# Performance work log

Hardware: AMD Instinct MI355X
Metric: run time of the kernel (lower is better)

## Reference

```python
import jax, jax.numpy as jnp
import numpy as np

EPS = 1e-6


def setup_inputs() -> dict:
    key = jax.random.key(0)
    kx, ky = jax.random.split(key)
    B, C, H, W = 8, 128, 48, 64
    x = jax.random.normal(kx, (B, C, H, W), dtype=jnp.float32)
    y = jax.random.normal(ky, (B, C, H, W), dtype=jnp.float32)
    return {"x": x, "y": y}


def reference(x, y):
    # x, y: (b, c, h, w)
    b, c, h, w = x.shape
    # torch: x.transpose(2,3).view(b,c,h*w) -> x flattened w-major,
    #        so output channel k = v*h + u corresponds to x[:, :, u, v].
    # corr5[b, v, u, i, j] = sum_c x[b,c,u,v] * y[b,c,i,j]
    corr = jnp.einsum('bcuv,bcij->bvuij', x, y)
    corr = corr.reshape(b, w * h, h, w)  # channel k = v*h + u
    # normalization: ReLU then L2-normalize over the h*w channel dim
    corr = jax.nn.relu(corr)
    norm = jnp.sqrt(jnp.sum(corr * corr, axis=1, keepdims=True) + EPS)
    return corr / norm
```

## Files before the change

### kernel.cpp

```cpp
#include <hip/hip_runtime.h>
#include <hip/hip_bf16.h>

#define NB 8
#define NC 128
#define NH 48
#define NW 64
#define NS 3072
#define EPSF 1e-6f

#define GLOBAL_AS __attribute__((address_space(1)))
#define LDS_AS __attribute__((address_space(3)))

typedef __bf16 bf16x8 __attribute__((ext_vector_type(8)));
typedef float f32x4 __attribute__((ext_vector_type(4)));

__device__ __forceinline__ unsigned short bf16_rtne(float f) {
  union { float f; unsigned u; } c;
  c.f = f;
  unsigned r = (c.u + 0x7fffu + ((c.u >> 16) & 1u)) >> 16;
  return (unsigned short)r;
}

__global__ __launch_bounds__(256) void transpose_both(
    const float* __restrict__ x, const float* __restrict__ y,
    __hip_bfloat16* __restrict__ AT, __hip_bfloat16* __restrict__ BT) {
  __shared__ float tile[32 * 129];
  const int id = blockIdx.x;
  const int b = id & 7;
  const int which = (id >> 3) & 1;
  const int f0 = (id >> 4) * 32;
  const float* src = which ? y : x;
  __hip_bfloat16* dst = which ? BT : AT;
  const int t = threadIdx.x;

  {
    const int fl = (t & 7) * 4, cg0 = t >> 3;
    const float* sp = src + (size_t)b * NC * NS + f0 + fl;
#pragma unroll
    for (int i = 0; i < 4; ++i) {
      int cg = cg0 + i * 32;
      f32x4 v = *(const f32x4*)(sp + (size_t)cg * NS);
      tile[(fl + 0) * 129 + cg] = v[0];
      tile[(fl + 1) * 129 + cg] = v[1];
      tile[(fl + 2) * 129 + cg] = v[2];
      tile[(fl + 3) * 129 + cg] = v[3];
    }
  }
  __syncthreads();
  {
    const int c4 = (t & 31) * 4, kl0 = t >> 5;
    unsigned short* dp = (unsigned short*)dst;
#pragma unroll
    for (int i = 0; i < 4; ++i) {
      int fl = kl0 + i * 8;
      int f = f0 + fl;
      int k = which ? f : ((f & 63) * NH + (f >> 6));
      f32x4 v = *(const f32x4*)&tile[fl * 129 + c4];
      ushort4 u4;
      u4.x = bf16_rtne(v[0]);
      u4.y = bf16_rtne(v[1]);
      u4.z = bf16_rtne(v[2]);
      u4.w = bf16_rtne(v[3]);
      *(ushort4*)(dp + ((size_t)b * NS + k) * NC + c4) = u4;
    }
  }
}

template <int CPW>
__device__ __forceinline__ void stage_tile(const char* gsrc, char* ldst,
                                           int wid, int lane) {
  const int lr = lane >> 4, lg = lane & 15;
#pragma unroll
  for (int i = 0; i < CPW; ++i) {
    int c = wid * CPW + i;
    int row = c * 4 + lr;
    int g = lg ^ (row & 7);
    __builtin_amdgcn_global_load_lds(
        (const GLOBAL_AS unsigned*)(gsrc + row * 256 + g * 16),
        (LDS_AS unsigned*)(ldst + c * 1024), 16, 0, 0);
  }
}

__global__ __launch_bounds__(256, 2) void corr_part_v2(
    const __hip_bfloat16* __restrict__ AT,
    const __hip_bfloat16* __restrict__ BT, float* __restrict__ part) {
  __shared__ char smem[65536];
  char* As = smem;
  char* Bs = smem + 32768;
  const int id = blockIdx.x;
  const int b = id & 7;
  const int tl = id >> 3;
  const int nt = tl >> 3;
  const int mg = tl & 7;
  const int t = threadIdx.x;
  const int lane = t & 63, wid = t >> 6;
  const int wm = wid >> 1, wn = wid & 1;
  const int l15 = lane & 15, kg = lane >> 4;

  const char* Ab = (const char*)(AT + ((size_t)b * NS + mg * 384) * NC);
  const char* Bg = (const char*)(BT + ((size_t)b * NS + nt * 128) * NC);

  stage_tile<8>(Bg, Bs, wid, lane);

  float cs[4] = {0.f, 0.f, 0.f, 0.f};
  const int rx = l15 & 7;
#pragma unroll 1
  for (int i = 0; i < 3; ++i) {
    stage_tile<8>(Ab + (size_t)i * 32768, As, wid, lane);
    asm volatile("s_waitcnt vmcnt(0)" ::: "memory");
    __builtin_amdgcn_sched_barrier(0);
    __builtin_amdgcn_s_barrier();

    f32x4 acc[4][4] = {};
#pragma unroll
    for (int kk = 0; kk < 4; ++kk) {
      int g = (kk * 4 + kg) ^ rx;
      bf16x8 a[4], bb[4];
#pragma unroll
      for (int mi = 0; mi < 4; ++mi)
        a[mi] = *(const bf16x8*)(As + (wm * 64 + mi * 16 + l15) * 256 + g * 16);
#pragma unroll
      for (int ni = 0; ni < 4; ++ni)
        bb[ni] =
            *(const bf16x8*)(Bs + (wn * 64 + ni * 16 + l15) * 256 + g * 16);
#pragma unroll
      for (int mi = 0; mi < 4; ++mi)
#pragma unroll
        for (int ni = 0; ni < 4; ++ni)
          acc[mi][ni] = __builtin_amdgcn_mfma_f32_16x16x32_bf16(
              a[mi], bb[ni], acc[mi][ni], 0, 0, 0);
    }
#pragma unroll
    for (int ni = 0; ni < 4; ++ni)
#pragma unroll
      for (int mi = 0; mi < 4; ++mi)
#pragma unroll
        for (int r = 0; r < 4; ++r) {
          float v = fmaxf(acc[mi][ni][r], 0.f);
          cs[ni] += v * v;
        }
    __builtin_amdgcn_s_barrier();
  }

#pragma unroll
  for (int ni = 0; ni < 4; ++ni) {
    cs[ni] += __shfl_xor(cs[ni], 16, 64);
    cs[ni] += __shfl_xor(cs[ni], 32, 64);
  }
  float* csum = (float*)smem;
  if (kg == 0) {
#pragma unroll
    for (int ni = 0; ni < 4; ++ni)
      csum[wm * 128 + wn * 64 + ni * 16 + l15] = cs[ni];
  }
  __syncthreads();
  if (t < 128) {
    float s = csum[t] + csum[128 + t];
    part[(size_t)mg * (NB * NS) + (size_t)b * NS + nt * 128 + t] = s;
  }
}

__global__ __launch_bounds__(256, 2) void corr_out(
    const __hip_bfloat16* __restrict__ AT,
    const __hip_bfloat16* __restrict__ BT, const float* __restrict__ part_in,
    float* __restrict__ out) {
  __shared__ char smem[66560];
  float* rnc = (float*)(smem + 65536);
  const int id = blockIdx.x;
  const int b = id & 7;
  const int tl = id >> 3;
  const int mt = tl / 24, nt = tl - mt * 24;
  const int t = threadIdx.x;
  const int lane = t & 63, wid = t >> 6;
  const int wm = wid >> 1, wn = wid & 1;
  const int l15 = lane & 15, kg = lane >> 4;

  const char* Ag = (const char*)(AT + ((size_t)b * NS + mt * 128) * NC);
  const char* Bg = (const char*)(BT + ((size_t)b * NS + nt * 128) * NC);
  stage_tile<8>(Ag, smem, wid, lane);
  stage_tile<8>(Bg, smem + 32768, wid, lane);
  if (t < 128) {
    float s = 0.f;
#pragma unroll
    for (int q = 0; q < 8; ++q)
      s += part_in[(size_t)q * (NB * NS) + (size_t)b * NS + nt * 128 + t];
    rnc[t] = rsqrtf(s + EPSF);
  }
  __syncthreads();

  f32x4 acc[4][4] = {};
  const int rx = l15 & 7;
#pragma unroll
  for (int kk = 0; kk < 4; ++kk) {
    int g = (kk * 4 + kg) ^ rx;
    bf16x8 a[4], bb[4];
#pragma unroll
    for (int mi = 0; mi < 4; ++mi)
      a[mi] = *(const bf16x8*)(smem + (wm * 64 + mi * 16 + l15) * 256 + g * 16);
#pragma unroll
    for (int ni = 0; ni < 4; ++ni)
      bb[ni] = *(const bf16x8*)(smem + 32768 +
                                (wn * 64 + ni * 16 + l15) * 256 + g * 16);
#pragma unroll
    for (int mi = 0; mi < 4; ++mi)
#pragma unroll
      for (int ni = 0; ni < 4; ++ni)
        acc[mi][ni] = __builtin_amdgcn_mfma_f32_16x16x32_bf16(
            a[mi], bb[ni], acc[mi][ni], 0, 0, 0);
  }

  float rnv[4];
#pragma unroll
  for (int ni = 0; ni < 4; ++ni) rnv[ni] = rnc[wn * 64 + ni * 16 + l15];
  __syncthreads();

  float* tf = (float*)smem;
#pragma unroll
  for (int mi = 0; mi < 4; ++mi)
#pragma unroll
    for (int ni = 0; ni < 4; ++ni)
#pragma unroll
      for (int r = 0; r < 4; ++r) {
        int row = wm * 64 + mi * 16 + kg * 4 + r;
        int col = wn * 64 + ni * 16 + l15;
        tf[row * 129 + col] = fmaxf(acc[mi][ni][r], 0.f) * rnv[ni];
      }
  __syncthreads();

  float* ob = out + (size_t)b * NS * NS + (size_t)(mt * 128) * NS + nt * 128;
  const int rsub = t >> 5, c4 = (t & 31) * 4;
#pragma unroll
  for (int it = 0; it < 16; ++it) {
    int row = it * 8 + rsub;
    f32x4 v = *(const f32x4*)&tf[row * 129 + c4];
    __builtin_nontemporal_store(v, (f32x4*)&ob[(size_t)row * NS + c4]);
  }
}

extern "C" void kernel_launch(void* const* d_in, const int* in_sizes, int n_in,
                              void* d_out, int out_size, void* d_ws,
                              size_t ws_size, hipStream_t stream) {
  const float* x = (const float*)d_in[0];
  const float* y = (const float*)d_in[1];
  float* out = (float*)d_out;
  char* ws = (char*)d_ws;

  const size_t AT_OFF = 0;
  const size_t BT_OFF = 6291456;
  const size_t PART_OFF = 12582912;
  const size_t NEED = 13369344;
  if (ws_size < NEED) return;

  __hip_bfloat16* AT = (__hip_bfloat16*)(ws + AT_OFF);
  __hip_bfloat16* BT = (__hip_bfloat16*)(ws + BT_OFF);
  float* part = (float*)(ws + PART_OFF);

  transpose_both<<<dim3(1536), dim3(256), 0, stream>>>(x, y, AT, BT);
  corr_part_v2<<<dim3(1536), dim3(256), 0, stream>>>(AT, BT, part);
  corr_out<<<dim3(4608), dim3(256), 0, stream>>>(AT, BT, part, out);
}
```

Baseline: 90.80 us.

## Keep B fragments in registers and store output directly from MFMA accumulators

In the partial-norm kernel, the B tile fragments are loaded from LDS into registers once and reused across all three A sub-tiles instead of being reloaded each iteration, and the A staging is restructured around that. In the output kernel, MFMA operands are swapped so each lane holds four consecutive output columns. The normalized result is then written straight to global memory as 16-byte stores, skipping the LDS transpose staging and its two barriers. This trades fully coalesced row-contiguous stores for fewer LDS round trips. The B-fragment caching also raises register pressure.

```diff
diff --git a/kernel.cpp b/kernel.cpp
--- a/kernel.cpp
+++ b/kernel.cpp
@@ -81,7 +81,7 @@
   }
 }
 
-__global__ __launch_bounds__(256, 2) void corr_part_v2(
+__global__ __launch_bounds__(256, 2) void corr_part_v4(
     const __hip_bfloat16* __restrict__ AT,
     const __hip_bfloat16* __restrict__ BT, float* __restrict__ part) {
   __shared__ char smem[65536];
@@ -101,34 +101,39 @@
   const char* Bg = (const char*)(BT + ((size_t)b * NS + nt * 128) * NC);
 
   stage_tile<8>(Bg, Bs, wid, lane);
+  stage_tile<8>(Ab, As, wid, lane);
+  asm volatile("s_waitcnt vmcnt(0)" ::: "memory");
+  __builtin_amdgcn_sched_barrier(0);
+  __builtin_amdgcn_s_barrier();
+
+  const int rx = l15 & 7;
+  bf16x8 bfrag[4][4];
+#pragma unroll
+  for (int kk = 0; kk < 4; ++kk) {
+    int g = (kk * 4 + kg) ^ rx;
+#pragma unroll
+    for (int ni = 0; ni < 4; ++ni)
+      bfrag[kk][ni] =
+          *(const bf16x8*)(Bs + (wn * 64 + ni * 16 + l15) * 256 + g * 16);
+  }
 
   float cs[4] = {0.f, 0.f, 0.f, 0.f};
-  const int rx = l15 & 7;
 #pragma unroll 1
   for (int i = 0; i < 3; ++i) {
-    stage_tile<8>(Ab + (size_t)i * 32768, As, wid, lane);
-    asm volatile("s_waitcnt vmcnt(0)" ::: "memory");
-    __builtin_amdgcn_sched_barrier(0);
-    __builtin_amdgcn_s_barrier();
-
     f32x4 acc[4][4] = {};
 #pragma unroll
     for (int kk = 0; kk < 4; ++kk) {
       int g = (kk * 4 + kg) ^ rx;
-      bf16x8 a[4], bb[4];
+      bf16x8 a[4];
 #pragma unroll
       for (int mi = 0; mi < 4; ++mi)
         a[mi] = *(const bf16x8*)(As + (wm * 64 + mi * 16 + l15) * 256 + g * 16);
 #pragma unroll
-      for (int ni = 0; ni < 4; ++ni)
-        bb[ni] =
-            *(const bf16x8*)(Bs + (wn * 64 + ni * 16 + l15) * 256 + g * 16);
-#pragma unroll
       for (int mi = 0; mi < 4; ++mi)
 #pragma unroll
         for (int ni = 0; ni < 4; ++ni)
           acc[mi][ni] = __builtin_amdgcn_mfma_f32_16x16x32_bf16(
-              a[mi], bb[ni], acc[mi][ni], 0, 0, 0);
+              a[mi], bfrag[kk][ni], acc[mi][ni], 0, 0, 0);
     }
 #pragma unroll
     for (int ni = 0; ni < 4; ++ni)
@@ -140,6 +145,12 @@
           cs[ni] += v * v;
         }
     __builtin_amdgcn_s_barrier();
+    if (i + 1 < 3) {
+      stage_tile<8>(Ab + (size_t)(i + 1) * 32768, As, wid, lane);
+      asm volatile("s_waitcnt vmcnt(0)" ::: "memory");
+      __builtin_amdgcn_sched_barrier(0);
+      __builtin_amdgcn_s_barrier();
+    }
   }
 
 #pragma unroll
@@ -160,7 +171,7 @@
   }
 }
 
-__global__ __launch_bounds__(256, 2) void corr_out(
+__global__ __launch_bounds__(256, 2) void corr_out_v3(
     const __hip_bfloat16* __restrict__ AT,
     const __hip_bfloat16* __restrict__ BT, const float* __restrict__ part_in,
     float* __restrict__ out) {
@@ -206,34 +217,28 @@
 #pragma unroll
       for (int ni = 0; ni < 4; ++ni)
         acc[mi][ni] = __builtin_amdgcn_mfma_f32_16x16x32_bf16(
-            a[mi], bb[ni], acc[mi][ni], 0, 0, 0);
-  }
-
-  float rnv[4];
-#pragma unroll
-  for (int ni = 0; ni < 4; ++ni) rnv[ni] = rnc[wn * 64 + ni * 16 + l15];
-  __syncthreads();
-
-  float* tf = (float*)smem;
-#pragma unroll
-  for (int mi = 0; mi < 4; ++mi)
-#pragma unroll
-    for (int ni = 0; ni < 4; ++ni)
-#pragma unroll
-      for (int r = 0; r < 4; ++r) {
-        int row = wm * 64 + mi * 16 + kg * 4 + r;
-        int col = wn * 64 + ni * 16 + l15;
-        tf[row * 129 + col] = fmaxf(acc[mi][ni][r], 0.f) * rnv[ni];
-      }
-  __syncthreads();
-
-  float* ob = out + (size_t)b * NS * NS + (size_t)(mt * 128) * NS + nt * 128;
-  const int rsub = t >> 5, c4 = (t & 31) * 4;
-#pragma unroll
-  for (int it = 0; it < 16; ++it) {
-    int row = it * 8 + rsub;
-    f32x4 v = *(const f32x4*)&tf[row * 129 + c4];
-    __builtin_nontemporal_store(v, (f32x4*)&ob[(size_t)row * NS + c4]);
+            bb[ni], a[mi], acc[mi][ni], 0, 0, 0);
+  }
+
+  f32x4 rnv[4];
+#pragma unroll
+  for (int ni = 0; ni < 4; ++ni)
+    rnv[ni] = *(const f32x4*)&rnc[wn * 64 + ni * 16 + kg * 4];
+
+  float* ob = out + (size_t)b * NS * NS + (size_t)(mt * 128 + wm * 64) * NS +
+              nt * 128 + wn * 64;
+#pragma unroll
+  for (int mi = 0; mi < 4; ++mi) {
+    size_t rowoff = (size_t)(mi * 16 + l15) * NS;
+#pragma unroll
+    for (int ni = 0; ni < 4; ++ni) {
+      f32x4 v;
+#pragma unroll
+      for (int r = 0; r < 4; ++r)
+        v[r] = fmaxf(acc[mi][ni][r], 0.f) * rnv[ni][r];
+      __builtin_nontemporal_store(
+          v, (f32x4*)&ob[rowoff + ni * 16 + kg * 4]);
+    }
   }
 }
 
@@ -256,6 +261,6 @@
   float* part = (float*)(ws + PART_OFF);
 
   transpose_both<<<dim3(1536), dim3(256), 0, stream>>>(x, y, AT, BT);
-  corr_part_v2<<<dim3(1536), dim3(256), 0, stream>>>(AT, BT, part);
-  corr_out<<<dim3(4608), dim3(256), 0, stream>>>(AT, BT, part, out);
-}
+  corr_part_v4<<<dim3(1536), dim3(256), 0, stream>>>(AT, BT, part);
+  corr_out_v3<<<dim3(4608), dim3(256), 0, stream>>>(AT, BT, part, out);
+}
```

Measured after the change: 119.4 us. +31.5%, slower.
